# Kernel optimization log

Measured on AMD Instinct MI355X. Metric: run time of the kernel, lower is better.

## Reference

```python
import jax, jax.numpy as jnp
import numpy as np

B, L, E, H = 4, 512, 2048, 32
S = E // H  # head_size = 64
EXTRA_MAA, EXTRA_DECAY = 32, 64
EPS = 1e-5


def setup_inputs() -> dict:
    key = jax.random.key(0)
    ks = jax.random.split(key, 24)
    rn = lambda k, shp, s=1.0: jax.random.normal(k, shp, dtype=jnp.float32) * s
    return dict(
        x=rn(ks[0], (B, L, E)),
        state=rn(ks[1], (B, 2 + S, E), 0.1),
        ln1_w=jnp.ones((E,), jnp.float32), ln1_b=jnp.zeros((E,), jnp.float32),
        ln2_w=jnp.ones((E,), jnp.float32), ln2_b=jnp.zeros((E,), jnp.float32),
        maa_x=rn(ks[2], (E,), 0.02),
        maa_w1=rn(ks[3], (E, 5 * EXTRA_MAA), 0.02),
        maa_w2=rn(ks[4], (5, EXTRA_MAA, E), 0.02),
        maa_stack=rn(ks[5], (5, E), 0.02),          # [k,w,v,r,g] time_maa vectors
        time_decay=rn(ks[6], (E,), 0.5),
        decay_w1=rn(ks[7], (E, EXTRA_DECAY), 0.02),
        decay_w2=rn(ks[8], (EXTRA_DECAY, E), 0.02),
        faaaa=rn(ks[9], (H, S), 0.1),
        Wr=rn(ks[10], (E, E), 0.02), Wk=rn(ks[11], (E, E), 0.02),
        Wv=rn(ks[12], (E, E), 0.02), Wg=rn(ks[13], (E, E), 0.02),
        Wo=rn(ks[14], (E, E), 0.02),
        gn_w=jnp.ones((E,), jnp.float32), gn_b=jnp.zeros((E,), jnp.float32),
        ffn_maa_k=rn(ks[15], (E,), 0.02), ffn_maa_r=rn(ks[16], (E,), 0.02),
        ffn_Wk=rn(ks[17], (E, E), 0.02), ffn_Wr=rn(ks[18], (E, E), 0.02),
        ffn_Wv=rn(ks[19], (E, E), 0.02),
        i=0,
    )


def _ln(x, w, b):
    m = jnp.mean(x, axis=-1, keepdims=True)
    v = jnp.mean((x - m) ** 2, axis=-1, keepdims=True)
    return (x - m) * jax.lax.rsqrt(v + EPS) * w + b


def _token_shift(xn, prev_row):
    # sx_lerp[t] = x[t-1] - x[t], with state row as x[-1]
    first = (prev_row - xn[:, 0])[:, None]
    rest = xn[:, :-1] - xn[:, 1:]
    return jnp.concatenate([first, rest], axis=1)


def reference(x, state, ln1_w, ln1_b, ln2_w, ln2_b, maa_x, maa_w1, maa_w2,
              maa_stack, time_decay, decay_w1, decay_w2, faaaa,
              Wr, Wk, Wv, Wg, Wo, gn_w, gn_b,
              ffn_maa_k, ffn_maa_r, ffn_Wk, ffn_Wr, ffn_Wv, i):
    b, l = x.shape[0], x.shape[1]
    i0 = (2 + S) * i + 0
    i1 = (2 + S) * i + 1

    # ---- time mixing (parallel) ----
    xn = _ln(x, ln1_w, ln1_b)
    sx = _token_shift(xn, state[:, i1])
    xxx = jnp.tanh((xn + sx * maa_x) @ maa_w1).reshape(b, l, 5, 1, EXTRA_MAA)
    xxx = jnp.matmul(xxx, maa_w2).reshape(b, l, 5, E)   # [B,L,5,E]
    x5 = xn[:, :, None] + sx[:, :, None] * (maa_stack + xxx)

    w = jnp.exp(-jnp.exp(time_decay + jnp.tanh(x5[:, :, 1] @ decay_w1) @ decay_w2))
    w = w.reshape(b, l, H, S)
    r = (x5[:, :, 3] @ Wr.T).reshape(b, l, H, S)
    k = (x5[:, :, 0] @ Wk.T).reshape(b, l, H, S)
    v = (x5[:, :, 2] @ Wv.T).reshape(b, l, H, S)
    g = jax.nn.silu(x5[:, :, 4] @ Wg.T)                 # [B,L,E]

    s0 = state[:, (2 + S) * i + 2:(2 + S) * (i + 1)].reshape(b, H, S, S)
    u = faaaa[None, :, :, None]                         # [1,H,S,1]

    def step(s, rkvw):
        r_t, k_t, v_t, w_t = rkvw                      # each [B,H,S]
        a = k_t[:, :, :, None] * v_t[:, :, None, :]    # [B,H,S,S] outer product
        out = jnp.einsum('bhk,bhkd->bhd', r_t, u * a + s)
        return a + w_t[:, :, :, None] * s, out

    xs = tuple(jnp.moveaxis(t, 1, 0) for t in (r, k, v, w))
    _, outs = jax.lax.scan(step, s0, xs)               # outs [L,B,H,S]
    att = jnp.moveaxis(outs, 0, 1).reshape(b, l, E)

    # group norm over each head's channels
    a4 = att.reshape(b, l, H, S)
    m = jnp.mean(a4, axis=-1, keepdims=True)
    var = jnp.mean((a4 - m) ** 2, axis=-1, keepdims=True)
    att = ((a4 - m) * jax.lax.rsqrt(var + EPS)).reshape(b, l, E) * gn_w + gn_b
    x = x + (att * g) @ Wo.T

    # ---- channel mixing (parallel) ----
    xn2 = _ln(x, ln2_w, ln2_b)
    sx2 = _token_shift(xn2, state[:, i0])
    xk = xn2 + sx2 * ffn_maa_k
    xr = xn2 + sx2 * ffn_maa_r
    rr = jax.nn.sigmoid(xr @ ffn_Wr.T)
    kk = jnp.square(jax.nn.relu(xk @ ffn_Wk.T))
    x = x + rr * (kk @ ffn_Wv.T)
    return x
```

## Files before the change

### kernel.cpp

```cpp
#include <hip/hip_runtime.h>

#define EE 2048
#define LL 512
#define BBATCH 4
#define HH 32
#define SS 64
#define EPSF 1e-5f
static constexpr size_t NEL = (size_t)BBATCH * LL * EE;

typedef __attribute__((ext_vector_type(8))) short short8;
typedef __attribute__((ext_vector_type(4))) float f32x4;

__device__ __forceinline__ unsigned short f2bf(float f) {
  union { float f; unsigned u; } x; x.f = f;
  return (unsigned short)((x.u + 0x7fffu + ((x.u >> 16) & 1u)) >> 16);
}

__device__ __forceinline__ void gload_lds16(const unsigned short* g, unsigned short* l) {
  __builtin_amdgcn_global_load_lds((const __attribute__((address_space(1))) void*)g,
                                   (__attribute__((address_space(3))) void*)l, 16, 0, 0);
}

template <int N>
__device__ __forceinline__ void wait_vmcnt_n() {
  if constexpr (N == 4) asm volatile("s_waitcnt vmcnt(4)" ::: "memory");
  else if constexpr (N == 6) asm volatile("s_waitcnt vmcnt(6)" ::: "memory");
  else if constexpr (N == 8) asm volatile("s_waitcnt vmcnt(8)" ::: "memory");
  else asm volatile("s_waitcnt vmcnt(0)" ::: "memory");
}

__device__ __forceinline__ void barrier_lgkm_only() {
  asm volatile("s_waitcnt lgkmcnt(0)" ::: "memory");
  __builtin_amdgcn_sched_barrier(0);
  __builtin_amdgcn_s_barrier();
}

struct CvArgs {
  const float* s[4];
  unsigned short* d[4];
};
__global__ void __launch_bounds__(256) f2bf_batch(CvArgs a, int n4) {
  int z = blockIdx.y;
  int idx = blockIdx.x * 256 + threadIdx.x;
  if (idx >= n4) return;
  float4 v = ((const float4*)a.s[z])[idx];
  ushort4 o;
  o.x = f2bf(v.x); o.y = f2bf(v.y); o.z = f2bf(v.z); o.w = f2bf(v.w);
  ((ushort4*)a.d[z])[idx] = o;
}

__global__ void __launch_bounds__(256) wprep_kernel(const float* __restrict__ w1,
                                                    const float* __restrict__ w2,
                                                    const float* __restrict__ d1,
                                                    const float* __restrict__ d2,
                                                    unsigned short* __restrict__ w1T,
                                                    unsigned short* __restrict__ w2cat,
                                                    unsigned short* __restrict__ dw1T,
                                                    unsigned short* __restrict__ dw2T) {
  const int N0 = 256 * 2048;
  const int N1 = 10240 * 160;
  const int N2 = 128 * 2048;
  const int N3 = 2048 * 128;
  int id = blockIdx.x * 256 + threadIdx.x;
  if (id < N0) {
    int n = id >> 11, k = id & 2047;
    float v = (n < 160) ? w1[(size_t)k * 160 + n] : 0.f;
    w1T[id] = f2bf(v);
    return;
  }
  id -= N0;
  if (id < N1) {
    int n = id / 160, kq = id - n * 160;
    int j = n >> 11, e = n & 2047;
    float v = ((kq >> 5) == j) ? w2[(size_t)kq * 2048 + e] : 0.f;
    w2cat[id] = f2bf(v);
    return;
  }
  id -= N1;
  if (id < N2) {
    int n = id >> 11, k = id & 2047;
    float v = (n < 64) ? d1[(size_t)k * 64 + n] : 0.f;
    dw1T[id] = f2bf(v);
    return;
  }
  id -= N2;
  if (id < N3) {
    int n = id >> 7, k = id & 127;
    float v = (k < 64) ? d2[(size_t)k * 2048 + n] : 0.f;
    dw2T[id] = f2bf(v);
  }
}

template <int SIDE>
__global__ void __launch_bounds__(256) ln_shift_kernel(
    const float* __restrict__ x, const float* __restrict__ state, const int* __restrict__ ip,
    const float* __restrict__ lnw, const float* __restrict__ lnb,
    const float* __restrict__ mA, const float* __restrict__ mB,
    float* __restrict__ xn_out, unsigned short* __restrict__ o1,
    float* __restrict__ sx_out, unsigned short* __restrict__ o2) {
  __shared__ float red[8];
  int tok = blockIdx.x;
  int b = tok >> 9, t = tok & 511;
  int tid = threadIdx.x;
  int e = tid * 8;
  size_t base = (size_t)tok * EE;
  float c[8], p[8];
  *(float4*)&c[0] = *(const float4*)&x[base + e];
  *(float4*)&c[4] = *(const float4*)&x[base + e + 4];
  bool hasp = (t != 0);
  if (hasp) {
    *(float4*)&p[0] = *(const float4*)&x[base - EE + e];
    *(float4*)&p[4] = *(const float4*)&x[base - EE + e + 4];
  } else {
    const float* srow = state + ((size_t)b * (2 + SS) + (size_t)(2 + SS) * (*ip) +
                                 (SIDE == 0 ? 1 : 0)) * EE;
    *(float4*)&p[0] = *(const float4*)&srow[e];
    *(float4*)&p[4] = *(const float4*)&srow[e + 4];
  }
  float sc = 0.f, sp = 0.f;
#pragma unroll
  for (int j = 0; j < 8; ++j) { sc += c[j]; sp += p[j]; }
#pragma unroll
  for (int off = 32; off >= 1; off >>= 1) {
    sc += __shfl_xor(sc, off);
    sp += __shfl_xor(sp, off);
  }
  if ((tid & 63) == 0) { red[tid >> 6] = sc; red[4 + (tid >> 6)] = sp; }
  __syncthreads();
  float mc = (red[0] + red[1] + red[2] + red[3]) * (1.f / EE);
  float mp = (red[4] + red[5] + red[6] + red[7]) * (1.f / EE);
  __syncthreads();
  float qc = 0.f, qp = 0.f;
#pragma unroll
  for (int j = 0; j < 8; ++j) {
    float dc = c[j] - mc, dp = p[j] - mp;
    qc += dc * dc; qp += dp * dp;
  }
#pragma unroll
  for (int off = 32; off >= 1; off >>= 1) {
    qc += __shfl_xor(qc, off);
    qp += __shfl_xor(qp, off);
  }
  if ((tid & 63) == 0) { red[tid >> 6] = qc; red[4 + (tid >> 6)] = qp; }
  __syncthreads();
  float rc = rsqrtf((red[0] + red[1] + red[2] + red[3]) * (1.f / EE) + EPSF);
  float rp = rsqrtf((red[4] + red[5] + red[6] + red[7]) * (1.f / EE) + EPSF);
  float wv[8], bv[8], av[8], bv2[8];
  *(float4*)&wv[0] = *(const float4*)&lnw[e];
  *(float4*)&wv[4] = *(const float4*)&lnw[e + 4];
  *(float4*)&bv[0] = *(const float4*)&lnb[e];
  *(float4*)&bv[4] = *(const float4*)&lnb[e + 4];
  *(float4*)&av[0] = *(const float4*)&mA[e];
  *(float4*)&av[4] = *(const float4*)&mA[e + 4];
  if (SIDE == 1) {
    *(float4*)&bv2[0] = *(const float4*)&mB[e];
    *(float4*)&bv2[4] = *(const float4*)&mB[e + 4];
  }
  float cn[8], sxv[8];
#pragma unroll
  for (int j = 0; j < 8; ++j) {
    float cnj = (c[j] - mc) * rc * wv[j] + bv[j];
    float pnj = hasp ? ((p[j] - mp) * rp * wv[j] + bv[j]) : p[j];
    cn[j] = cnj;
    sxv[j] = pnj - cnj;
  }
  if constexpr (SIDE == 0) {
    *(float4*)&xn_out[base + e] = *(float4*)&cn[0];
    *(float4*)&xn_out[base + e + 4] = *(float4*)&cn[4];
    *(float4*)&sx_out[base + e] = *(float4*)&sxv[0];
    *(float4*)&sx_out[base + e + 4] = *(float4*)&sxv[4];
    ushort4 xo0, xo1;
    xo0.x = f2bf(cn[0] + sxv[0] * av[0]); xo0.y = f2bf(cn[1] + sxv[1] * av[1]);
    xo0.z = f2bf(cn[2] + sxv[2] * av[2]); xo0.w = f2bf(cn[3] + sxv[3] * av[3]);
    xo1.x = f2bf(cn[4] + sxv[4] * av[4]); xo1.y = f2bf(cn[5] + sxv[5] * av[5]);
    xo1.z = f2bf(cn[6] + sxv[6] * av[6]); xo1.w = f2bf(cn[7] + sxv[7] * av[7]);
    *(ushort4*)&o1[base + e] = xo0;
    *(ushort4*)&o1[base + e + 4] = xo1;
  } else {
    ushort4 k0, k1, r0, r1;
    k0.x = f2bf(cn[0] + sxv[0] * av[0]); k0.y = f2bf(cn[1] + sxv[1] * av[1]);
    k0.z = f2bf(cn[2] + sxv[2] * av[2]); k0.w = f2bf(cn[3] + sxv[3] * av[3]);
    k1.x = f2bf(cn[4] + sxv[4] * av[4]); k1.y = f2bf(cn[5] + sxv[5] * av[5]);
    k1.z = f2bf(cn[6] + sxv[6] * av[6]); k1.w = f2bf(cn[7] + sxv[7] * av[7]);
    r0.x = f2bf(cn[0] + sxv[0] * bv2[0]); r0.y = f2bf(cn[1] + sxv[1] * bv2[1]);
    r0.z = f2bf(cn[2] + sxv[2] * bv2[2]); r0.w = f2bf(cn[3] + sxv[3] * bv2[3]);
    r1.x = f2bf(cn[4] + sxv[4] * bv2[4]); r1.y = f2bf(cn[5] + sxv[5] * bv2[5]);
    r1.z = f2bf(cn[6] + sxv[6] * bv2[6]); r1.w = f2bf(cn[7] + sxv[7] * bv2[7]);
    *(ushort4*)&o1[base + e] = k0;
    *(ushort4*)&o1[base + e + 4] = k1;
    *(ushort4*)&o2[base + e] = r0;
    *(ushort4*)&o2[base + e + 4] = r1;
  }
}

template <int ROWS, int BK, int NT>
__device__ __forceinline__ void stage_mat(const unsigned short* __restrict__ base, int ld,
                                          int k0, unsigned short* dst) {
  constexpr int GPR = BK / 8;
  constexpr int L = ROWS * GPR / NT;
  int tid = threadIdx.x;
#pragma unroll
  for (int r = 0; r < L; ++r) {
    int g = r * NT + tid;
    int row = g / GPR, p = g & (GPR - 1);
    int lg = p ^ (row & (GPR - 1));
    gload_lds16(base + (size_t)row * ld + k0 + lg * 8, &dst[g * 8]);
  }
}

template <int BM, int BN, int BK, int NT, int WM, int WN, bool SPLIT = false>
__device__ __forceinline__ void gemm_core(const unsigned short* __restrict__ A, int lda,
                                          const unsigned short* __restrict__ W, int ldw,
                                          int K, int bm, int bn, unsigned short* AsAll,
                                          unsigned short* BsAll,
                                          f32x4 (&acc)[BM / WM / 16][BN / WN / 16],
                                          int& m0o, int& n0o) {
  constexpr int FM = BM / WM / 16, FN = BN / WN / 16, KS = BK / 32;
  constexpr int GPR = BK / 8;
  constexpr int NLD = (BM + BN) * GPR / NT;
  int tid = threadIdx.x;
  int wave = tid >> 6, lane = tid & 63;
  int wm = wave / WN, wn = wave % WN;
  const unsigned short* Abase = A + (size_t)bm * BM * lda;
  const unsigned short* Bbase = W + (size_t)bn * BN * ldw;
  const int T = K / BK;
  stage_mat<BM, BK, NT>(Abase, lda, 0, AsAll);
  stage_mat<BN, BK, NT>(Bbase, ldw, 0, BsAll);
  {
    int k1 = (T > 1) ? BK : 0;
    stage_mat<BM, BK, NT>(Abase, lda, k1, AsAll + BM * BK);
    stage_mat<BN, BK, NT>(Bbase, ldw, k1, BsAll + BN * BK);
  }
  int q = lane >> 4;
  int rA = wm * (BM / WM) + (lane & 15);
  int rB = wn * (BN / WN) + (lane & 15);
  int xrA = rA & (GPR - 1), xrB = rB & (GPR - 1);
  for (int t = 0; t < T; ++t) {
    unsigned short* As = AsAll + (t & 1) * (BM * BK);
    unsigned short* Bs = BsAll + (t & 1) * (BN * BK);
    wait_vmcnt_n<NLD>();
    __builtin_amdgcn_s_barrier();
    __builtin_amdgcn_sched_barrier(0);
    short8 av[KS][FM], bv[KS][FN];
#pragma unroll
    for (int ks = 0; ks < KS; ++ks) {
#pragma unroll
      for (int f = 0; f < FM; f++) {
        int p = (ks * 4 + q) ^ xrA;
        av[ks][f] = *(const short8*)&As[(rA + f * 16) * BK + p * 8];
      }
#pragma unroll
      for (int f = 0; f < FN; f++) {
        int p = (ks * 4 + q) ^ xrB;
        bv[ks][f] = *(const short8*)&Bs[(rB + f * 16) * BK + p * 8];
      }
    }
    if constexpr (SPLIT && KS >= 2) {
#pragma unroll
      for (int fm = 0; fm < FM; fm++)
#pragma unroll
        for (int fn = 0; fn < FN; fn++)
          acc[fm][fn] = __builtin_amdgcn_mfma_f32_16x16x32_bf16(av[0][fm], bv[0][fn],
                                                                acc[fm][fn], 0, 0, 0);
    }
    asm volatile("s_waitcnt lgkmcnt(0)" ::: "memory");
    __builtin_amdgcn_sched_barrier(0);
    __builtin_amdgcn_s_barrier();
    int tn = t + 2;
    if (tn >= T) tn -= T;
    stage_mat<BM, BK, NT>(Abase, lda, tn * BK, As);
    stage_mat<BN, BK, NT>(Bbase, ldw, tn * BK, Bs);
    __builtin_amdgcn_s_setprio(1);
    if constexpr (SPLIT && KS >= 2) {
#pragma unroll
      for (int ks = 1; ks < KS; ++ks)
#pragma unroll
        for (int fm = 0; fm < FM; fm++)
#pragma unroll
          for (int fn = 0; fn < FN; fn++)
            acc[fm][fn] = __builtin_amdgcn_mfma_f32_16x16x32_bf16(av[ks][fm], bv[ks][fn],
                                                                  acc[fm][fn], 0, 0, 0);
    } else {
#pragma unroll
      for (int ks = 0; ks < KS; ++ks)
#pragma unroll
        for (int fm = 0; fm < FM; fm++)
#pragma unroll
          for (int fn = 0; fn < FN; fn++)
            acc[fm][fn] = __builtin_amdgcn_mfma_f32_16x16x32_bf16(av[ks][fm], bv[ks][fn],
                                                                  acc[fm][fn], 0, 0, 0);
    }
    __builtin_amdgcn_s_setprio(0);
  }
  m0o = bm * BM + wm * (BM / WM);
  n0o = bn * BN + wn * (BN / WN);
}

template <int FM, int FN, typename F>
__device__ __forceinline__ void epi_loop(f32x4 (&acc)[FM][FN], int m0, int n0, F f) {
  int lane = threadIdx.x & 63;
  int rl = (lane >> 4) * 4, cl = lane & 15;
#pragma unroll
  for (int fm = 0; fm < FM; fm++)
#pragma unroll
    for (int fn = 0; fn < FN; fn++)
#pragma unroll
      for (int q = 0; q < 4; q++)
        f(m0 + fm * 16 + rl + q, n0 + fn * 16 + cl, acc[fm][fn][q]);
}

template <int MODE, int BM, int BN, int BK>
__global__ void __launch_bounds__(256) gemm_bt(const unsigned short* __restrict__ A, int lda,
                                               const unsigned short* __restrict__ W, int ldw,
                                               int K, int NB, void* __restrict__ Cout, int ldc,
                                               const float* __restrict__ p1,
                                               const float* __restrict__ p2,
                                               const float* __restrict__ p3) {
  __shared__ __align__(16) unsigned short As[2 * BM * BK];
  __shared__ __align__(16) unsigned short Bs[2 * BN * BK];
  int nwg = gridDim.x, bid = blockIdx.x;
  int qd = nwg >> 3;
  int wg = (bid & 7) * qd + (bid >> 3);
  int bm = wg / NB, bn = wg - bm * NB;
  f32x4 acc[BM / 32][BN / 32] = {};
  int m0, n0;
  gemm_core<BM, BN, BK, 256, 2, 2>(A, lda, W, ldw, K, bm, bn, As, Bs, acc, m0, n0);
  epi_loop(acc, m0, n0, [&](int m, int n, float val) {
    size_t o = (size_t)m * ldc + n;
    if constexpr (MODE == 2) {
      ((float*)Cout)[o] = p1[o] + val;
    } else if constexpr (MODE == 3) {
      ((float*)Cout)[o] = p1[o] + val * (1.f / (1.f + expf(-p2[o])));
    } else if constexpr (MODE == 5) {
      ((unsigned short*)Cout)[o] = f2bf(tanhf(val));
    } else if constexpr (MODE == 6) {
      ((float*)Cout)[o] = expf(-expf(p1[n] + val));
    } else {
      int j = n >> 11, e = n & 2047;
      size_t oe = (size_t)m * EE + e;
      float xv = p1[oe];
      float sv = p2[oe];
      float st = p3[(size_t)j * EE + e];
      ((unsigned short*)Cout)[(size_t)j * NEL + oe] = f2bf(xv + sv * (st + val));
    }
  });
}

struct Proj4Args {
  const unsigned short* A[4];
  const unsigned short* W[4];
  float* C[4];
};
__global__ void __launch_bounds__(512, 1) gemm_proj4(Proj4Args args) {
  __shared__ __align__(16) unsigned short As[2 * 256 * 64];
  __shared__ __align__(16) unsigned short Bs[2 * 256 * 64];
  int bid = blockIdx.x;
  int xcd = bid & 7;
  int z = xcd >> 1;
  int tile = ((xcd & 1) << 5) + (bid >> 3);
  int bm = tile >> 3, bn = tile & 7;
  f32x4 acc[8][4] = {};
  int m0, n0;
  gemm_core<256, 256, 64, 512, 2, 4, true>(args.A[z], EE, args.W[z], EE, EE, bm, bn, As, Bs,
                                           acc, m0, n0);
  float* C = args.C[z];
  bool silu = (z == 3);
  epi_loop(acc, m0, n0, [&](int m, int n, float val) {
    size_t o = (size_t)m * EE + n;
    C[o] = silu ? (val / (1.f + expf(-val))) : val;
  });
}

__global__ void __launch_bounds__(256) gemm_ffn2(const unsigned short* A0,
                                                 const unsigned short* A1,
                                                 const unsigned short* W0,
                                                 const unsigned short* W1, float* C0,
                                                 unsigned short* C1) {
  __shared__ __align__(16) unsigned short As[2 * 128 * 64];
  __shared__ __align__(16) unsigned short Bs[2 * 128 * 64];
  int bid = blockIdx.x;
  int xcd = bid & 7;
  int z = xcd >> 2;
  int tile = ((xcd & 3) << 6) + (bid >> 3);
  int bm = tile >> 4, bn = tile & 15;
  f32x4 acc[4][4] = {};
  int m0, n0;
  gemm_core<128, 128, 64, 256, 2, 2>(z ? A1 : A0, EE, z ? W1 : W0, EE, EE, bm, bn, As, Bs,
                                     acc, m0, n0);
  epi_loop(acc, m0, n0, [&](int m, int n, float val) {
    size_t o = (size_t)m * EE + n;
    if (z == 0) {
      C0[o] = val;
    } else {
      float rv = fmaxf(val, 0.f);
      C1[o] = f2bf(rv * rv);
    }
  });
}

#define GS 16
__global__ void __launch_bounds__(512) scan_kernel(const float* __restrict__ r,
                                                   const float* __restrict__ k,
                                                   const float* __restrict__ v,
                                                   const float* __restrict__ w,
                                                   const float* __restrict__ state,
                                                   const float* __restrict__ faaaa,
                                                   const int* __restrict__ ip,
                                                   float* __restrict__ att) {
  __shared__ float bufAll[2][GS * 224];
  __shared__ float part[2][GS][8][34];
  int blk = blockIdx.x;
  int bh = blk >> 1, dh = blk & 1;
  int b = bh >> 5, h = bh & 31;
  int tid = threadIdx.x, wv = tid >> 6, lane = tid & 63;
  int d32 = lane & 31;
  int k0w = wv * 8 + (lane >> 5) * 4;
  int dfull = dh * 32 + d32;
  int ii = *ip;
  const float* sb = state + ((size_t)b * (2 + SS) + (size_t)(2 + SS) * ii + 2) * EE;
  float s_[4], u_[4];
#pragma unroll
  for (int q = 0; q < 4; ++q) {
    int kk_ = k0w + q;
    s_[q] = sb[(size_t)(2 * h + (kk_ >> 5)) * EE + (kk_ & 31) * 64 + dfull];
    u_[q] = faaaa[h * 64 + kk_];
  }
  size_t base = (size_t)b * LL * EE + (size_t)h * 64;
  int i0 = tid;
  int row0 = i0 / 56, j0 = i0 - row0 * 56;
  const float* a0p; int off0, gc0;
  if (j0 < 16) { a0p = r; off0 = j0 * 4; gc0 = j0 * 4; }
  else if (j0 < 32) { a0p = k; off0 = 64 + (j0 - 16) * 4; gc0 = (j0 - 16) * 4; }
  else if (j0 < 48) { a0p = w; off0 = 128 + (j0 - 32) * 4; gc0 = (j0 - 32) * 4; }
  else { a0p = v; off0 = 192 + (j0 - 48) * 4; gc0 = dh * 32 + (j0 - 48) * 4; }
  const float* lsrc0 = a0p + base + (size_t)row0 * EE + gc0;
  int loff0 = row0 * 224 + off0;
  bool has1 = (tid < 384);
  int i1 = tid + 512;
  int row1 = i1 / 56, j1 = i1 - row1 * 56;
  const float* a1p; int off1, gc1;
  if (j1 < 16) { a1p = r; off1 = j1 * 4; gc1 = j1 * 4; }
  else if (j1 < 32) { a1p = k; off1 = 64 + (j1 - 16) * 4; gc1 = (j1 - 16) * 4; }
  else if (j1 < 48) { a1p = w; off1 = 128 + (j1 - 32) * 4; gc1 = (j1 - 32) * 4; }
  else { a1p = v; off1 = 192 + (j1 - 48) * 4; gc1 = dh * 32 + (j1 - 48) * 4; }
  const float* lsrc1 = a1p + base + (size_t)row1 * EE + gc1;
  int loff1 = row1 * 224 + off1;

  auto compute = [&](const float* buf, float (*pt)[8][34]) {
#pragma unroll
    for (int t = 0; t < GS; ++t) {
      const float* rowp = buf + t * 224;
      float vv = rowp[192 + d32];
      float acc = 0.f;
#pragma unroll
      for (int q = 0; q < 4; ++q) {
        float rk = rowp[k0w + q];
        float kk2 = rowp[64 + k0w + q];
        float wk = rowp[128 + k0w + q];
        float a = kk2 * vv;
        acc = fmaf(rk, fmaf(u_[q], a, s_[q]), acc);
        s_[q] = fmaf(wk, s_[q], a);
      }
      acc += __shfl_xor(acc, 32);
      if (lane < 32) pt[t][wv][d32] = acc;
    }
  };
  auto reduce = [&](int g, float (*pt)[8][34]) {
    int tt = tid >> 5, dd = tid & 31;
    float tot = pt[tt][0][dd] + pt[tt][1][dd] + pt[tt][2][dd] + pt[tt][3][dd] +
                pt[tt][4][dd] + pt[tt][5][dd] + pt[tt][6][dd] + pt[tt][7][dd];
    att[base + (size_t)(g * GS + tt) * EE + dh * 32 + dd] = tot;
  };

  *(float4*)&bufAll[0][loff0] = *(const float4*)lsrc0;
  if (has1) *(float4*)&bufAll[0][loff1] = *(const float4*)lsrc1;
  float4 ra0, ra1, rb0, rb1;
  ra0 = *(const float4*)(lsrc0 + (size_t)GS * EE);
  if (has1) ra1 = *(const float4*)(lsrc1 + (size_t)GS * EE);
  barrier_lgkm_only();
  for (int gg = 0; gg < 32; gg += 2) {
    if (gg + 2 < 32) {
      rb0 = *(const float4*)(lsrc0 + (size_t)(gg + 2) * GS * EE);
      if (has1) rb1 = *(const float4*)(lsrc1 + (size_t)(gg + 2) * GS * EE);
    }
    compute(bufAll[0], part[0]);
    *(float4*)&bufAll[1][loff0] = ra0;
    if (has1) *(float4*)&bufAll[1][loff1] = ra1;
    barrier_lgkm_only();
    reduce(gg, part[0]);
    if (gg + 3 < 32) {
      ra0 = *(const float4*)(lsrc0 + (size_t)(gg + 3) * GS * EE);
      if (has1) ra1 = *(const float4*)(lsrc1 + (size_t)(gg + 3) * GS * EE);
    }
    compute(bufAll[1], part[1]);
    if (gg + 2 < 32) {
      *(float4*)&bufAll[0][loff0] = rb0;
      if (has1) *(float4*)&bufAll[0][loff1] = rb1;
    }
    barrier_lgkm_only();
    reduce(gg + 1, part[1]);
  }
}

__global__ void __launch_bounds__(256) gn_gate_kernel(const float* __restrict__ att,
                                                      const float* __restrict__ g,
                                                      const float* __restrict__ gnw,
                                                      const float* __restrict__ gnb,
                                                      unsigned short* __restrict__ attg) {
  int tok = blockIdx.x, tid = threadIdx.x;
  int h = tid >> 3, j = tid & 7;
  size_t base = (size_t)tok * EE + h * 64 + j * 8;
  int e = h * 64 + j * 8;
  float4 a0 = *(const float4*)&att[base];
  float4 a1 = *(const float4*)&att[base + 4];
  float s = a0.x + a0.y + a0.z + a0.w + a1.x + a1.y + a1.z + a1.w;
  s += __shfl_xor(s, 1); s += __shfl_xor(s, 2); s += __shfl_xor(s, 4);
  float mean = s * (1.f / 64.f);
  float d, q = 0.f;
  d = a0.x - mean; q += d * d; d = a0.y - mean; q += d * d;
  d = a0.z - mean; q += d * d; d = a0.w - mean; q += d * d;
  d = a1.x - mean; q += d * d; d = a1.y - mean; q += d * d;
  d = a1.z - mean; q += d * d; d = a1.w - mean; q += d * d;
  q += __shfl_xor(q, 1); q += __shfl_xor(q, 2); q += __shfl_xor(q, 4);
  float rstd = rsqrtf(q * (1.f / 64.f) + EPSF);
  float4 w0 = *(const float4*)&gnw[e], w1 = *(const float4*)&gnw[e + 4];
  float4 b0 = *(const float4*)&gnb[e], b1 = *(const float4*)&gnb[e + 4];
  float4 g0 = *(const float4*)&g[base], g1 = *(const float4*)&g[base + 4];
  ushort4 o0, o1;
  o0.x = f2bf(((a0.x - mean) * rstd * w0.x + b0.x) * g0.x);
  o0.y = f2bf(((a0.y - mean) * rstd * w0.y + b0.y) * g0.y);
  o0.z = f2bf(((a0.z - mean) * rstd * w0.z + b0.z) * g0.z);
  o0.w = f2bf(((a0.w - mean) * rstd * w0.w + b0.w) * g0.w);
  o1.x = f2bf(((a1.x - mean) * rstd * w1.x + b1.x) * g1.x);
  o1.y = f2bf(((a1.y - mean) * rstd * w1.y + b1.y) * g1.y);
  o1.z = f2bf(((a1.z - mean) * rstd * w1.z + b1.z) * g1.z);
  o1.w = f2bf(((a1.w - mean) * rstd * w1.w + b1.w) * g1.w);
  *(ushort4*)&attg[base] = o0;
  *(ushort4*)&attg[base + 4] = o1;
}

extern "C" void kernel_launch(void* const* d_in, const int* in_sizes, int n_in,
                              void* d_out, int out_size, void* d_ws, size_t ws_size,
                              hipStream_t stream) {
  const float* x = (const float*)d_in[0];
  const float* state = (const float*)d_in[1];
  const float* ln1_w = (const float*)d_in[2];
  const float* ln1_b = (const float*)d_in[3];
  const float* ln2_w = (const float*)d_in[4];
  const float* ln2_b = (const float*)d_in[5];
  const float* maa_x = (const float*)d_in[6];
  const float* maa_w1 = (const float*)d_in[7];
  const float* maa_w2 = (const float*)d_in[8];
  const float* maa_stack = (const float*)d_in[9];
  const float* time_decay = (const float*)d_in[10];
  const float* decay_w1 = (const float*)d_in[11];
  const float* decay_w2 = (const float*)d_in[12];
  const float* faaaa = (const float*)d_in[13];
  const float* Wr = (const float*)d_in[14];
  const float* Wk = (const float*)d_in[15];
  const float* Wv = (const float*)d_in[16];
  const float* Wg = (const float*)d_in[17];
  const float* Wo = (const float*)d_in[18];
  const float* gn_w = (const float*)d_in[19];
  const float* gn_b = (const float*)d_in[20];
  const float* ffn_maa_k = (const float*)d_in[21];
  const float* ffn_maa_r = (const float*)d_in[22];
  const float* fWk = (const float*)d_in[23];
  const float* fWr = (const float*)d_in[24];
  const float* fWv = (const float*)d_in[25];
  const int* ip = (const int*)d_in[26];

  char* ws = (char*)d_ws;
  const size_t MB1 = 1024 * 1024;
  unsigned short* WB0 = (unsigned short*)ws;
  unsigned short* WB1 = (unsigned short*)(ws + 8 * MB1);
  float* xn = (float*)(ws + 16 * MB1);
  unsigned short* x5b = (unsigned short*)(ws + 32 * MB1);
  float* wbuf = (float*)(ws + 72 * MB1);
  float* rbuf = (float*)(ws + 88 * MB1);
  float* kbuf = (float*)(ws + 104 * MB1);
  float* vbuf = (float*)(ws + 120 * MB1);
  float* gbuf = (float*)(ws + 136 * MB1);
  char* smalls = ws + 152 * MB1;
  unsigned short* th = (unsigned short*)smalls;
  unsigned short* w1T = (unsigned short*)(smalls + 1 * MB1);
  unsigned short* w2cat = (unsigned short*)(smalls + 2 * MB1);
  unsigned short* dw1T = (unsigned short*)(smalls + 5376 * 1024);
  unsigned short* dw2T = (unsigned short*)(smalls + 5888 * 1024);
  unsigned short* dt = (unsigned short*)(smalls + 6400 * 1024);

  unsigned short* xxm = (unsigned short*)wbuf;
  float* sx = gbuf;
  float* att = xn;
  unsigned short* WB2 = (unsigned short*)xn;
  unsigned short* WB3 = WB2 + NEL;
  unsigned short* attg = x5b;
  unsigned short* xkb = x5b;
  unsigned short* fWvB = x5b + 1 * NEL;
  unsigned short* xrb = x5b + 2 * NEL;
  unsigned short* kkb = x5b + 3 * NEL;
  unsigned short* fWkB = x5b + 4 * NEL;
  float* rrraw = wbuf;

  const int thr = 256;
  const int nconv = (int)(NEL / 4);

  ln_shift_kernel<0><<<BBATCH * LL, thr, 0, stream>>>(x, state, ip, ln1_w, ln1_b, maa_x,
                                                      nullptr, xn, xxm, sx, nullptr);
  wprep_kernel<<<10496, thr, 0, stream>>>(maa_w1, maa_w2, decay_w1, decay_w2, w1T, w2cat,
                                          dw1T, dw2T);
  gemm_bt<5, 64, 64, 64><<<128, thr, 0, stream>>>(xxm, 2048, w1T, 2048, 2048, 4, th, 256,
                                                  nullptr, nullptr, nullptr);
  gemm_bt<7, 128, 128, 32><<<1280, thr, 0, stream>>>(th, 256, w2cat, 160, 160, 80, x5b, 0,
                                                     xn, sx, maa_stack);
  gemm_bt<5, 64, 64, 64><<<64, thr, 0, stream>>>(x5b + 1 * NEL, 2048, dw1T, 2048, 2048, 2,
                                                 dt, 128, nullptr, nullptr, nullptr);
  gemm_bt<6, 128, 128, 64><<<256, thr, 0, stream>>>(dt, 128, dw2T, 128, 128, 16, wbuf, 2048,
                                                    time_decay, nullptr, nullptr);
  {
    CvArgs ca;
    ca.s[0] = Wk; ca.d[0] = WB0;
    ca.s[1] = Wv; ca.d[1] = WB1;
    ca.s[2] = Wr; ca.d[2] = WB2;
    ca.s[3] = Wg; ca.d[3] = WB3;
    f2bf_batch<<<dim3(4096, 4), thr, 0, stream>>>(ca, nconv);
  }
  {
    Proj4Args pa;
    pa.A[0] = x5b + 0 * NEL; pa.W[0] = WB0; pa.C[0] = kbuf;
    pa.A[1] = x5b + 2 * NEL; pa.W[1] = WB1; pa.C[1] = vbuf;
    pa.A[2] = x5b + 3 * NEL; pa.W[2] = WB2; pa.C[2] = rbuf;
    pa.A[3] = x5b + 4 * NEL; pa.W[3] = WB3; pa.C[3] = gbuf;
    gemm_proj4<<<256, 512, 0, stream>>>(pa);
  }
  {
    CvArgs cb;
    cb.s[0] = Wo; cb.d[0] = WB0;
    cb.s[1] = fWr; cb.d[1] = WB1;
    cb.s[2] = fWk; cb.d[2] = fWkB;
    cb.s[3] = fWv; cb.d[3] = fWvB;
    f2bf_batch<<<dim3(4096, 4), thr, 0, stream>>>(cb, nconv);
  }
  scan_kernel<<<256, 512, 0, stream>>>(rbuf, kbuf, vbuf, wbuf, state, faaaa, ip, att);
  gn_gate_kernel<<<BBATCH * LL, thr, 0, stream>>>(att, gbuf, gn_w, gn_b, attg);
  gemm_bt<2, 128, 64, 64><<<512, thr, 0, stream>>>(attg, 2048, WB0, 2048, 2048, 32,
                                                   (float*)d_out, 2048, x, nullptr, nullptr);
  ln_shift_kernel<1><<<BBATCH * LL, thr, 0, stream>>>((const float*)d_out, state, ip, ln2_w,
                                                      ln2_b, ffn_maa_k, ffn_maa_r, nullptr,
                                                      xkb, nullptr, xrb);
  gemm_ffn2<<<512, thr, 0, stream>>>(xrb, xkb, WB1, fWkB, rrraw, kkb);
  gemm_bt<3, 128, 64, 64><<<512, thr, 0, stream>>>(kkb, 2048, fWvB, 2048, 2048, 32,
                                                   (float*)d_out, 2048, (const float*)d_out,
                                                   rrraw, nullptr);
}
```

Baseline: 410.0 us.

## Co-schedule weight bf16 conversions inside decay GEMM and scan kernels

The standalone f2bf_batch launches are removed. The first weight conversion now runs as extra blocks of a combined decay-GEMM kernel, and the second runs as extra blocks of the scan kernel. The aim is to overlap memory-bound conversion with the low-occupancy scan (256 blocks) and the small GEMM, and to drop two launches. The cost is that the scan kernel's 512-thread blocks and large LDS footprint now apply to the conversion blocks, which may limit co-residency, and block ordering is left to the hardware scheduler.

```diff
diff --git a/kernel.cpp b/kernel.cpp
--- a/kernel.cpp
+++ b/kernel.cpp
@@ -39,15 +39,6 @@
   const float* s[4];
   unsigned short* d[4];
 };
-__global__ void __launch_bounds__(256) f2bf_batch(CvArgs a, int n4) {
-  int z = blockIdx.y;
-  int idx = blockIdx.x * 256 + threadIdx.x;
-  if (idx >= n4) return;
-  float4 v = ((const float4*)a.s[z])[idx];
-  ushort4 o;
-  o.x = f2bf(v.x); o.y = f2bf(v.y); o.z = f2bf(v.z); o.w = f2bf(v.w);
-  ((ushort4*)a.d[z])[idx] = o;
-}
 
 __global__ void __launch_bounds__(256) wprep_kernel(const float* __restrict__ w1,
                                                     const float* __restrict__ w2,
@@ -333,8 +324,6 @@
       ((float*)Cout)[o] = p1[o] + val * (1.f / (1.f + expf(-p2[o])));
     } else if constexpr (MODE == 5) {
       ((unsigned short*)Cout)[o] = f2bf(tanhf(val));
-    } else if constexpr (MODE == 6) {
-      ((float*)Cout)[o] = expf(-expf(p1[n] + val));
     } else {
       int j = n >> 11, e = n & 2047;
       size_t oe = (size_t)m * EE + e;
@@ -343,6 +332,32 @@
       float st = p3[(size_t)j * EE + e];
       ((unsigned short*)Cout)[(size_t)j * NEL + oe] = f2bf(xv + sv * (st + val));
     }
+  });
+}
+
+__global__ void __launch_bounds__(256) wgemm_f2bf(const unsigned short* __restrict__ dt,
+                                                  const unsigned short* __restrict__ dw2T,
+                                                  const float* __restrict__ td,
+                                                  float* __restrict__ wout, CvArgs cv) {
+  __shared__ __align__(16) unsigned short As[2 * 128 * 64];
+  __shared__ __align__(16) unsigned short Bs[2 * 128 * 64];
+  if (blockIdx.x >= 256) {
+    int fid = blockIdx.x - 256;
+    int z = fid >> 12;
+    size_t i = ((size_t)(fid & 4095)) * 256 + threadIdx.x;
+    float4 v = ((const float4*)cv.s[z])[i];
+    ushort4 o;
+    o.x = f2bf(v.x); o.y = f2bf(v.y); o.z = f2bf(v.z); o.w = f2bf(v.w);
+    ((ushort4*)cv.d[z])[i] = o;
+    return;
+  }
+  int wg = blockIdx.x;
+  int bm = wg >> 4, bn = wg & 15;
+  f32x4 acc[4][4] = {};
+  int m0, n0;
+  gemm_core<128, 128, 64, 256, 2, 2>(dt, 128, dw2T, 128, 128, bm, bn, As, Bs, acc, m0, n0);
+  epi_loop(acc, m0, n0, [&](int m, int n, float val) {
+    wout[(size_t)m * EE + n] = expf(-expf(td[n] + val));
   });
 }
 
@@ -399,16 +414,35 @@
 }
 
 #define GS 16
-__global__ void __launch_bounds__(512) scan_kernel(const float* __restrict__ r,
-                                                   const float* __restrict__ k,
-                                                   const float* __restrict__ v,
-                                                   const float* __restrict__ w,
-                                                   const float* __restrict__ state,
-                                                   const float* __restrict__ faaaa,
-                                                   const int* __restrict__ ip,
-                                                   float* __restrict__ att) {
+__global__ void __launch_bounds__(512) scan_f2bf(const float* __restrict__ r,
+                                                 const float* __restrict__ k,
+                                                 const float* __restrict__ v,
+                                                 const float* __restrict__ w,
+                                                 const float* __restrict__ state,
+                                                 const float* __restrict__ faaaa,
+                                                 const int* __restrict__ ip,
+                                                 float* __restrict__ att, CvArgs cv) {
   __shared__ float bufAll[2][GS * 224];
   __shared__ float part[2][GS][8][34];
+  if (blockIdx.x >= 256) {
+    int fid = blockIdx.x - 256;
+    int z = fid >> 10;
+    size_t base_i = ((size_t)(fid & 1023)) * 512 + threadIdx.x;
+    {
+      float4 x0 = ((const float4*)cv.s[z])[base_i];
+      ushort4 o;
+      o.x = f2bf(x0.x); o.y = f2bf(x0.y); o.z = f2bf(x0.z); o.w = f2bf(x0.w);
+      ((ushort4*)cv.d[z])[base_i] = o;
+    }
+    {
+      size_t i2 = base_i + 524288;
+      float4 x1 = ((const float4*)cv.s[z])[i2];
+      ushort4 o;
+      o.x = f2bf(x1.x); o.y = f2bf(x1.y); o.z = f2bf(x1.z); o.w = f2bf(x1.w);
+      ((ushort4*)cv.d[z])[i2] = o;
+    }
+    return;
+  }
   int blk = blockIdx.x;
   int bh = blk >> 1, dh = blk & 1;
   int b = bh >> 5, h = bh & 31;
@@ -603,7 +637,6 @@
   float* rrraw = wbuf;
 
   const int thr = 256;
-  const int nconv = (int)(NEL / 4);
 
   ln_shift_kernel<0><<<BBATCH * LL, thr, 0, stream>>>(x, state, ip, ln1_w, ln1_b, maa_x,
                                                       nullptr, xn, xxm, sx, nullptr);
@@ -615,15 +648,13 @@
                                                      xn, sx, maa_stack);
   gemm_bt<5, 64, 64, 64><<<64, thr, 0, stream>>>(x5b + 1 * NEL, 2048, dw1T, 2048, 2048, 2,
                                                  dt, 128, nullptr, nullptr, nullptr);
-  gemm_bt<6, 128, 128, 64><<<256, thr, 0, stream>>>(dt, 128, dw2T, 128, 128, 16, wbuf, 2048,
-                                                    time_decay, nullptr, nullptr);
   {
     CvArgs ca;
     ca.s[0] = Wk; ca.d[0] = WB0;
     ca.s[1] = Wv; ca.d[1] = WB1;
     ca.s[2] = Wr; ca.d[2] = WB2;
     ca.s[3] = Wg; ca.d[3] = WB3;
-    f2bf_batch<<<dim3(4096, 4), thr, 0, stream>>>(ca, nconv);
+    wgemm_f2bf<<<256 + 16384, thr, 0, stream>>>(dt, dw2T, time_decay, wbuf, ca);
   }
   {
     Proj4Args pa;
@@ -639,9 +670,9 @@
     cb.s[1] = fWr; cb.d[1] = WB1;
     cb.s[2] = fWk; cb.d[2] = fWkB;
     cb.s[3] = fWv; cb.d[3] = fWvB;
-    f2bf_batch<<<dim3(4096, 4), thr, 0, stream>>>(cb, nconv);
-  }
-  scan_kernel<<<256, 512, 0, stream>>>(rbuf, kbuf, vbuf, wbuf, state, faaaa, ip, att);
+    scan_f2bf<<<256 + 4096, 512, 0, stream>>>(rbuf, kbuf, vbuf, wbuf, state, faaaa, ip,
+                                              att, cb);
+  }
   gn_gate_kernel<<<BBATCH * LL, thr, 0, stream>>>(att, gbuf, gn_w, gn_b, attg);
   gemm_bt<2, 128, 64, 64><<<512, thr, 0, stream>>>(attg, 2048, WB0, 2048, 2048, 32,
                                                    (float*)d_out, 2048, x, nullptr, nullptr);
```

Result: faster. 397.5 us (median of 2 runs) (-3.1%).
